# Kernel optimization log

Measured on AMD Instinct MI355X. Metric: run time of the kernel, lower is better.

The kernel has to match this reference:

```python
import jax, jax.numpy as jnp
import numpy as np
import math

B, S, D = 16, 1024, 512

def setup_inputs() -> dict:
    key = jax.random.key(0)
    ks = jax.random.split(key, 7)
    s = 1.0 / math.sqrt(D)
    return {
        "features_4h": jax.random.normal(ks[0], (B, S, D), jnp.float32),
        "features_1d": jax.random.normal(ks[1], (B, S, D), jnp.float32),
        "features_1w": jax.random.normal(ks[2], (B, S, D), jnp.float32),
        "Wq": jax.random.normal(ks[3], (D, D), jnp.float32) * s,
        "bq": jnp.zeros((D,), jnp.float32),
        "Wk": jax.random.normal(ks[4], (D, D), jnp.float32) * s,
        "bk": jnp.zeros((D,), jnp.float32),
        "Wv": jax.random.normal(ks[5], (D, D), jnp.float32) * s,
        "bv": jnp.zeros((D,), jnp.float32),
        "tf_weights": jnp.ones((3,), jnp.float32),
    }

def reference(features_4h, features_1d, features_1w, Wq, bq, Wk, bk, Wv, bv, tf_weights):
    # stacked: [B, T=3, S, D]
    stacked = jnp.stack([features_4h, features_1d, features_1w], axis=1)
    scale = 1.0 / math.sqrt(stacked.shape[-1])
    # torch nn.Linear: x @ W.T + b
    Q = jnp.einsum("btsd,ed->btse", stacked, Wq) + bq
    K = jnp.einsum("btsd,ed->btse", stacked, Wk) + bk
    V = jnp.einsum("btsd,ed->btse", stacked, Wv) + bv
    scores = jnp.einsum("btqd,btkd->btqk", Q, K) * scale  # [B,T,S,S]
    attn = jax.nn.softmax(scores, axis=-1)
    attended = jnp.einsum("btqk,btkd->btqd", attn, V)  # [B,T,S,D]
    w = jax.nn.softmax(tf_weights, axis=0)  # [T]
    return jnp.einsum("btsd,t->bsd", attended, w)  # [B,S,D]
```

## Files before the change

kernel.cpp:

```cpp
#include <hip/hip_runtime.h>
#include <cstdint>

typedef __bf16 bf16x8 __attribute__((ext_vector_type(8)));
typedef unsigned short u16x8 __attribute__((ext_vector_type(8)));
typedef float f32x4 __attribute__((ext_vector_type(4)));


__device__ __forceinline__ unsigned short f2bf(float x){
  unsigned u = __float_as_uint(x);
  u += 0x7fffu + ((u >> 16) & 1u);
  return (unsigned short)(u >> 16);
}

__device__ __forceinline__ void gload16(const void* src, void* dst){
  auto g = reinterpret_cast<const uint32_t __attribute__((address_space(1)))*>(
             reinterpret_cast<uintptr_t>(src));
  auto l = reinterpret_cast<uint32_t __attribute__((address_space(3)))*>(
             reinterpret_cast<uintptr_t>(dst));
  __builtin_amdgcn_global_load_lds(g, l, 16, 0, 0);
}

__device__ __forceinline__ void stage_tile(const unsigned short* __restrict__ g, size_t ld,
                                           unsigned short* l, int tid){
  #pragma unroll
  for (int i = 0; i < 4; ++i){
    int j = i * 256 + tid;
    int r = j >> 3, cc = j & 7;
    int c = cc ^ (r & 7);
    gload16(g + (size_t)r * ld + c * 8, l + (size_t)(i * 256 + (tid & 192)) * 8);
  }
}

__device__ __forceinline__ bf16x8 frag_at(const unsigned short* l, int row, int kch){
  int ch = kch ^ (row & 7);
  return *(const bf16x8*)(l + (row << 6) + (ch << 3));
}

__global__ void k_prep(const float* __restrict__ Wq, const float* __restrict__ Wk,
                       const float* __restrict__ Wv, const float* __restrict__ bq,
                       unsigned short* __restrict__ WqT, unsigned short* __restrict__ WkT,
                       unsigned short* __restrict__ Wv16, float* __restrict__ w1){
  __shared__ float sh[64 * 65];
  const int bi = blockIdx.x;
  const int tid = threadIdx.x;
  if (bi < 128){
    const float* src = (bi & 64) ? Wk : Wq;
    unsigned short* dst = (bi & 64) ? WkT : WqT;
    int te = (bi >> 3) & 7, td = bi & 7;
    #pragma unroll
    for (int i = 0; i < 4; ++i){
      int q = i * 256 + tid;
      int r = q >> 4, c4 = q & 15;
      f32x4 v = *(const f32x4*)(src + (size_t)(te * 64 + r) * 512 + td * 64 + c4 * 4);
      sh[r * 65 + c4 * 4 + 0] = v[0]; sh[r * 65 + c4 * 4 + 1] = v[1];
      sh[r * 65 + c4 * 4 + 2] = v[2]; sh[r * 65 + c4 * 4 + 3] = v[3];
    }
    __syncthreads();
    #pragma unroll
    for (int i = 0; i < 2; ++i){
      int q = i * 256 + tid;
      int r = q >> 3, c8 = q & 7;
      u16x8 o;
      #pragma unroll
      for (int j = 0; j < 8; ++j) o[j] = f2bf(sh[(c8 * 8 + j) * 65 + r]);
      *(u16x8*)(dst + (size_t)(td * 64 + r) * 512 + te * 64 + c8 * 8) = o;
    }
  } else if (bi < 256){
    size_t e = ((size_t)(bi - 128) * 256 + tid) * 8;
    f32x4 v0 = *(const f32x4*)(Wv + e), v1 = *(const f32x4*)(Wv + e + 4);
    u16x8 o;
    o[0] = f2bf(v0[0]); o[1] = f2bf(v0[1]); o[2] = f2bf(v0[2]); o[3] = f2bf(v0[3]);
    o[4] = f2bf(v1[0]); o[5] = f2bf(v1[1]); o[6] = f2bf(v1[2]); o[7] = f2bf(v1[3]);
    *(u16x8*)(Wv16 + e) = o;
  } else {
    int d = (bi - 256) * 64 + (tid & 63);
    int eq = tid >> 6;
    float s = 0.f;
    #pragma unroll 8
    for (int e = eq * 128; e < eq * 128 + 128; ++e) s += Wk[(size_t)e * 512 + d] * bq[e];
    sh[eq * 64 + (tid & 63)] = s;
    __syncthreads();
    if (eq == 0)
      w1[d] = (sh[tid] + sh[64 + tid] + sh[128 + tid] + sh[192 + tid]) * 0.04419417382415922f;
  }
}

__global__ void k_conv_feat(const float* __restrict__ f0, const float* __restrict__ f1,
                            const float* __restrict__ f2, const float* __restrict__ w1,
                            unsigned short* __restrict__ Xb, float* __restrict__ vcol){
  size_t i = (size_t)blockIdx.x * blockDim.x + threadIdx.x;
  size_t e = i * 8;
  size_t bt = e >> 19;
  size_t rest = e & ((1u << 19) - 1);
  int b = (int)(bt / 3), t = (int)(bt % 3);
  const float* src = (t == 0 ? f0 : (t == 1 ? f1 : f2)) + ((size_t)b << 19) + rest;
  f32x4 v0 = *(const f32x4*)(src);
  f32x4 v1 = *(const f32x4*)(src + 4);
  u16x8 o;
  o[0] = f2bf(v0[0]); o[1] = f2bf(v0[1]); o[2] = f2bf(v0[2]); o[3] = f2bf(v0[3]);
  o[4] = f2bf(v1[0]); o[5] = f2bf(v1[1]); o[6] = f2bf(v1[2]); o[7] = f2bf(v1[3]);
  *(u16x8*)(Xb + e) = o;
  int l = threadIdx.x & 63;
  f32x4 wa = *(const f32x4*)(w1 + l * 8);
  f32x4 wb = *(const f32x4*)(w1 + l * 8 + 4);
  float p = v0[0]*wa[0] + v0[1]*wa[1] + v0[2]*wa[2] + v0[3]*wa[3]
          + v1[0]*wb[0] + v1[1]*wb[1] + v1[2]*wb[2] + v1[3]*wb[3];
  p += __shfl_xor(p, 1);  p += __shfl_xor(p, 2);  p += __shfl_xor(p, 4);
  p += __shfl_xor(p, 8);  p += __shfl_xor(p, 16); p += __shfl_xor(p, 32);
  if (l == 0) vcol[i >> 6] = p;
}

template<int MODE>
__global__ __launch_bounds__(256, 2)
void k_gemm_proj(const unsigned short* __restrict__ A, const unsigned short* __restrict__ Bm,
                 const float* __restrict__ bias, unsigned short* __restrict__ C, int N, float scale){
  __shared__ __align__(16) unsigned short Al[2][8192];
  __shared__ __align__(16) unsigned short Bl[2][8192];
  const int tid = threadIdx.x;
  const int l  = tid & 63;
  const int wid = tid >> 6;
  const int lr = l & 15;
  const int lg = l >> 4;
  const int cpx = gridDim.x >> 3;
  const int wg = (blockIdx.x & 7) * cpx + (blockIdx.x >> 3);
  const int nbc = N >> 7;
  int rb, cb;
  if (MODE == 1){ cb = wg >> 2; rb = wg & 3; }
  else          { rb = wg / nbc; cb = wg % nbc; }
  const unsigned short* Ab = A + (size_t)rb * 128 * 512;
  const unsigned short* Bb = Bm + (size_t)cb * 128 * 512;

  const f32x4 zero4 = {0.f, 0.f, 0.f, 0.f};
  f32x4 acc[4][4];
  #pragma unroll
  for (int i = 0; i < 4; ++i)
    #pragma unroll
    for (int j = 0; j < 4; ++j) acc[i][j] = zero4;

  stage_tile(Ab, 512, &Al[0][0], tid);
  stage_tile(Bb, 512, &Bl[0][0], tid);
  __syncthreads();

  const int wr = wid >> 1, wc = wid & 1;

  for (int kb = 0; kb < 8; ++kb){
    const int cur = kb & 1;
    if (kb < 7){
      stage_tile(Ab + (kb + 1) * 64, 512, &Al[cur ^ 1][0], tid);
      stage_tile(Bb + (kb + 1) * 64, 512, &Bl[cur ^ 1][0], tid);
    }
    #pragma unroll
    for (int ks = 0; ks < 2; ++ks){
      bf16x8 af[4], bf[4];
      #pragma unroll
      for (int i = 0; i < 4; ++i) af[i] = frag_at(&Al[cur][0], wr * 64 + i * 16 + lr, ks * 4 + lg);
      #pragma unroll
      for (int j = 0; j < 4; ++j) bf[j] = frag_at(&Bl[cur][0], wc * 64 + j * 16 + lr, ks * 4 + lg);
      #pragma unroll
      for (int i = 0; i < 4; ++i)
        #pragma unroll
        for (int j = 0; j < 4; ++j)
          acc[i][j] = __builtin_amdgcn_mfma_f32_16x16x32_bf16(af[i], bf[j], acc[i][j], 0, 0, 0);
    }
    __syncthreads();
  }

  unsigned short* eL = &Al[0][0];
  #pragma unroll
  for (int j = 0; j < 4; ++j){
    int lcol = wc * 64 + j * 16 + lr;
    float bc = (MODE == 0) ? (bias ? bias[cb * 128 + lcol] : 0.f) : 0.f;
    #pragma unroll
    for (int i = 0; i < 4; ++i){
      int lrow0 = wr * 64 + i * 16 + lg * 4;
      #pragma unroll
      for (int r = 0; r < 4; ++r){
        float v;
        if (MODE == 0) v = (acc[i][j][r] + bc) * scale;
        else           v = acc[i][j][r] + bias[rb * 128 + lrow0 + r];
        eL[(lrow0 + r) * 128 + lcol] = f2bf(v);
      }
    }
  }
  __syncthreads();
  if (MODE == 0){
    #pragma unroll
    for (int q = 0; q < 8; ++q){
      int idx = q * 256 + tid;
      int row = idx >> 4, col = (idx & 15) * 8;
      *(u16x8*)(&C[(size_t)(rb * 128 + row) * N + cb * 128 + col]) =
          *(const u16x8*)(&eL[row * 128 + col]);
    }
  } else {
    size_t base = ((size_t)(cb >> 3) << 19) + (size_t)(cb & 7) * 128;
    #pragma unroll
    for (int q = 0; q < 8; ++q){
      int idx = q * 256 + tid;
      int row = idx >> 4, col = (idx & 15) * 8;
      *(u16x8*)(&C[base + ((size_t)(rb * 128 + row) << 10) + col]) =
          *(const u16x8*)(&eL[row * 128 + col]);
    }
  }
}

__global__ __launch_bounds__(256, 2)
void k_gemm_qk(const unsigned short* __restrict__ Gb, const unsigned short* __restrict__ Xb,
               unsigned short* __restrict__ S, int bt0){
  __shared__ __align__(16) unsigned short Al[2][8192];
  __shared__ __align__(16) unsigned short Bl[2][8192];
  const int tid = threadIdx.x;
  const int l  = tid & 63;
  const int wid = tid >> 6;
  const int lr = l & 15;
  const int lg = l >> 4;
  const int cpx = gridDim.x >> 3;
  const int wg = (blockIdx.x & 7) * cpx + (blockIdx.x >> 3);
  const int btl = wg >> 6;
  const int bt = bt0 + btl;
  const int tile = wg & 63;
  const int rb = tile >> 3, cb = tile & 7;
  const unsigned short* Ab = Gb + ((size_t)bt << 19) + (size_t)rb * 128 * 512;
  const unsigned short* Bb = Xb + ((size_t)bt << 19) + (size_t)cb * 128 * 512;
  unsigned short* Cb = S + ((size_t)btl << 20);

  const f32x4 zero4 = {0.f, 0.f, 0.f, 0.f};
  f32x4 acc[4][4];
  #pragma unroll
  for (int i = 0; i < 4; ++i)
    #pragma unroll
    for (int j = 0; j < 4; ++j) acc[i][j] = zero4;

  stage_tile(Ab, 512, &Al[0][0], tid);
  stage_tile(Bb, 512, &Bl[0][0], tid);
  __syncthreads();

  const int wr = wid >> 1, wc = wid & 1;

  for (int kb = 0; kb < 8; ++kb){
    const int cur = kb & 1;
    if (kb < 7){
      stage_tile(Ab + (kb + 1) * 64, 512, &Al[cur ^ 1][0], tid);
      stage_tile(Bb + (kb + 1) * 64, 512, &Bl[cur ^ 1][0], tid);
    }
    #pragma unroll
    for (int ks = 0; ks < 2; ++ks){
      bf16x8 af[4], bf[4];
      #pragma unroll
      for (int i = 0; i < 4; ++i) af[i] = frag_at(&Al[cur][0], wr * 64 + i * 16 + lr, ks * 4 + lg);
      #pragma unroll
      for (int j = 0; j < 4; ++j) bf[j] = frag_at(&Bl[cur][0], wc * 64 + j * 16 + lr, ks * 4 + lg);
      #pragma unroll
      for (int i = 0; i < 4; ++i)
        #pragma unroll
        for (int j = 0; j < 4; ++j)
          acc[i][j] = __builtin_amdgcn_mfma_f32_16x16x32_bf16(af[i], bf[j], acc[i][j], 0, 0, 0);
    }
    __syncthreads();
  }

  unsigned short* eL = &Al[0][0];
  #pragma unroll
  for (int j = 0; j < 4; ++j){
    int lcol = wc * 64 + j * 16 + lr;
    #pragma unroll
    for (int i = 0; i < 4; ++i){
      int lrow0 = wr * 64 + i * 16 + lg * 4;
      #pragma unroll
      for (int r = 0; r < 4; ++r){
        _Float16 h = (_Float16)acc[i][j][r];
        eL[(lrow0 + r) * 128 + lcol] = __builtin_bit_cast(unsigned short, h);
      }
    }
  }
  __syncthreads();
  #pragma unroll
  for (int q = 0; q < 8; ++q){
    int idx = q * 256 + tid;
    int row = idx >> 4, col = (idx & 15) * 8;
    *(u16x8*)(&Cb[((size_t)(rb * 128 + row) << 10) + cb * 128 + col]) =
        *(const u16x8*)(&eL[row * 128 + col]);
  }
}

__global__ __launch_bounds__(256)
void k_softmax(unsigned short* __restrict__ S, const float* __restrict__ vcol,
               const float* __restrict__ tfw, int bt0){
  const int wid = threadIdx.x >> 6, l = threadIdx.x & 63;
  const size_t row = (size_t)blockIdx.x * 4 + wid;
  const int bt = bt0 + (int)(row >> 10);
  const int t = bt % 3;
  float t0 = tfw[0], t1 = tfw[1], t2 = tfw[2];
  float tm = fmaxf(t0, fmaxf(t1, t2));
  float e0 = __expf(t0 - tm), e1 = __expf(t1 - tm), e2 = __expf(t2 - tm);
  float w = (t == 0 ? e0 : (t == 1 ? e1 : e2)) / (e0 + e1 + e2);

  const float* vr = vcol + ((size_t)bt << 10) + l * 16;
  unsigned short* rp = S + (row << 10) + l * 16;
  u16x8 a = *(const u16x8*)rp;
  u16x8 b = *(const u16x8*)(rp + 8);
  f32x4 va0 = *(const f32x4*)(vr), va1 = *(const f32x4*)(vr + 4);
  f32x4 va2 = *(const f32x4*)(vr + 8), va3 = *(const f32x4*)(vr + 12);
  float x[16];
  #pragma unroll
  for (int j = 0; j < 8; ++j){
    x[j]     = (float)__builtin_bit_cast(_Float16, (unsigned short)a[j]);
    x[8 + j] = (float)__builtin_bit_cast(_Float16, (unsigned short)b[j]);
  }
  x[0] += va0[0]; x[1] += va0[1]; x[2]  += va0[2]; x[3]  += va0[3];
  x[4] += va1[0]; x[5] += va1[1]; x[6]  += va1[2]; x[7]  += va1[3];
  x[8] += va2[0]; x[9] += va2[1]; x[10] += va2[2]; x[11] += va2[3];
  x[12]+= va3[0]; x[13]+= va3[1]; x[14] += va3[2]; x[15] += va3[3];
  float m = x[0];
  #pragma unroll
  for (int j = 1; j < 16; ++j) m = fmaxf(m, x[j]);
  m = fmaxf(m, __shfl_xor(m, 1));
  m = fmaxf(m, __shfl_xor(m, 2));
  m = fmaxf(m, __shfl_xor(m, 4));
  m = fmaxf(m, __shfl_xor(m, 8));
  m = fmaxf(m, __shfl_xor(m, 16));
  m = fmaxf(m, __shfl_xor(m, 32));
  float s = 0.f;
  #pragma unroll
  for (int j = 0; j < 16; ++j){ x[j] = __expf(x[j] - m); s += x[j]; }
  s += __shfl_xor(s, 1);
  s += __shfl_xor(s, 2);
  s += __shfl_xor(s, 4);
  s += __shfl_xor(s, 8);
  s += __shfl_xor(s, 16);
  s += __shfl_xor(s, 32);
  float sc = w / s;
  u16x8 oa, ob;
  #pragma unroll
  for (int j = 0; j < 8; ++j){
    oa[j] = f2bf(x[j] * sc);
    ob[j] = f2bf(x[8 + j] * sc);
  }
  *(u16x8*)rp = oa;
  *(u16x8*)(rp + 8) = ob;
}

__global__ __launch_bounds__(256, 2)
void k_gemm_pv(const unsigned short* __restrict__ P, const unsigned short* __restrict__ Vt,
               float* __restrict__ out, int b0){
  __shared__ __align__(16) unsigned short Al[2][8192];
  __shared__ __align__(16) unsigned short Bl[2][8192];
  const int tid = threadIdx.x;
  const int l  = tid & 63;
  const int wid = tid >> 6;
  const int lr = l & 15;
  const int lg = l >> 4;
  const int cpx = gridDim.x >> 3;
  const int wg = (blockIdx.x & 7) * cpx + (blockIdx.x >> 3);
  const int bl = wg >> 5;
  const int b = b0 + bl;
  const int tile = wg & 31;
  const int rb = tile >> 2, cb = tile & 3;

  const f32x4 zero4 = {0.f, 0.f, 0.f, 0.f};
  f32x4 acc[4][4];
  #pragma unroll
  for (int i = 0; i < 4; ++i)
    #pragma unroll
    for (int j = 0; j < 4; ++j) acc[i][j] = zero4;

  {
    const unsigned short* Ab = P  + ((size_t)(bl * 3) << 20) + (size_t)rb * 128 * 1024;
    const unsigned short* Bb = Vt + ((size_t)(b * 3) << 19) + (size_t)cb * 128 * 1024;
    stage_tile(Ab, 1024, &Al[0][0], tid);
    stage_tile(Bb, 1024, &Bl[0][0], tid);
  }
  __syncthreads();

  const int wr = wid >> 1, wc = wid & 1;

  #pragma unroll 2
  for (int kb = 0; kb < 48; ++kb){
    const int cur = kb & 1;
    if (kb < 47){
      int kn = kb + 1;
      int t = kn >> 4, kk = kn & 15;
      const unsigned short* Ab = P  + ((size_t)(bl * 3 + t) << 20) + (size_t)rb * 128 * 1024 + kk * 64;
      const unsigned short* Bb = Vt + ((size_t)(b * 3 + t) << 19) + (size_t)cb * 128 * 1024 + kk * 64;
      stage_tile(Ab, 1024, &Al[cur ^ 1][0], tid);
      stage_tile(Bb, 1024, &Bl[cur ^ 1][0], tid);
    }
    #pragma unroll
    for (int ks = 0; ks < 2; ++ks){
      bf16x8 af[4], bf[4];
      #pragma unroll
      for (int i = 0; i < 4; ++i) af[i] = frag_at(&Al[cur][0], wr * 64 + i * 16 + lr, ks * 4 + lg);
      #pragma unroll
      for (int j = 0; j < 4; ++j) bf[j] = frag_at(&Bl[cur][0], wc * 64 + j * 16 + lr, ks * 4 + lg);
      #pragma unroll
      for (int i = 0; i < 4; ++i)
        #pragma unroll
        for (int j = 0; j < 4; ++j)
          acc[i][j] = __builtin_amdgcn_mfma_f32_16x16x32_bf16(af[i], bf[j], acc[i][j], 0, 0, 0);
    }
    __syncthreads();
  }

  float* ob = out + ((size_t)b << 19);
  #pragma unroll
  for (int j = 0; j < 4; ++j){
    int col = cb * 128 + wc * 64 + j * 16 + lr;
    #pragma unroll
    for (int i = 0; i < 4; ++i){
      int row0 = rb * 128 + wr * 64 + i * 16 + lg * 4;
      #pragma unroll
      for (int r = 0; r < 4; ++r){
        ob[((size_t)(row0 + r) << 9) + col] = acc[i][j][r];
      }
    }
  }
}

extern "C" void kernel_launch(void* const* d_in, const int* in_sizes, int n_in,
                              void* d_out, int out_size, void* d_ws, size_t ws_size,
                              hipStream_t stream){
  (void)in_sizes; (void)n_in; (void)out_size;
  const float* f4h = (const float*)d_in[0];
  const float* f1d = (const float*)d_in[1];
  const float* f1w = (const float*)d_in[2];
  const float* Wq  = (const float*)d_in[3];
  const float* bq  = (const float*)d_in[4];
  const float* Wk  = (const float*)d_in[5];
  const float* bk  = (const float*)d_in[6];
  const float* Wv  = (const float*)d_in[7];
  const float* bv  = (const float*)d_in[8];
  const float* tfw = (const float*)d_in[9];
  (void)bk;
  float* out = (float*)d_out;

  const size_t N48 = (size_t)48 * 1024 * 512;
  unsigned short* Gb  = (unsigned short*)d_ws;
  unsigned short* Xb  = Gb + N48;
  unsigned short* Vt  = Xb + N48;
  float*          vcol = (float*)(Vt + N48);
  unsigned short* WqT = (unsigned short*)(vcol + 49152);
  unsigned short* WkT = WqT + 262144;
  unsigned short* Wv16= WkT + 262144;
  unsigned short* Mt  = Wv16 + 262144;
  float*          w1  = (float*)(Mt + 262144);
  unsigned short* Sb  = WqT;

  const float SC = 0.04419417382415922f;
  const size_t base = 3 * N48 * 2 + 49152 * 4;
  const size_t s_full = (size_t)48 * 1024 * 1024 * 2;

  k_prep<<<264, 256, 0, stream>>>(Wq, Wk, Wv, bq, WqT, WkT, Wv16, w1);
  k_conv_feat<<<12288, 256, 0, stream>>>(f4h, f1d, f1w, w1, Xb, vcol);
  k_gemm_proj<0><<<16, 256, 0, stream>>>(WkT, WqT, nullptr, Mt, 512, SC);
  k_gemm_proj<0><<<1536, 256, 0, stream>>>(Xb, Mt, nullptr, Gb, 512, 1.0f);
  k_gemm_proj<1><<<1536, 256, 0, stream>>>(Wv16, Xb, bv, Vt, 49152, 1.0f);

  if (ws_size >= base + 2048 + s_full){
    k_gemm_qk<<<3072, 256, 0, stream>>>(Gb, Xb, Sb, 0);
    k_softmax<<<12288, 256, 0, stream>>>(Sb, vcol, tfw, 0);
    k_gemm_pv<<<512, 256, 0, stream>>>(Sb, Vt, out, 0);
  } else {
    for (int h = 0; h < 2; ++h){
      int bt0 = h * 24;
      k_gemm_qk<<<1536, 256, 0, stream>>>(Gb, Xb, Sb, bt0);
      k_softmax<<<6144, 256, 0, stream>>>(Sb, vcol, tfw, bt0);
      k_gemm_pv<<<256, 256, 0, stream>>>(Sb, Vt, out, h * 8);
    }
  }
}
```

Measured before the change: 268.7 us.

## Defer V projection until after attention by reassociating P·(X·Wv) as (P·X)·Wv

```diff
diff --git a/kernel.cpp b/kernel.cpp
--- a/kernel.cpp
+++ b/kernel.cpp
@@ -3,6 +3,7 @@
 
 typedef __bf16 bf16x8 __attribute__((ext_vector_type(8)));
 typedef unsigned short u16x8 __attribute__((ext_vector_type(8)));
+typedef unsigned short u16x4 __attribute__((ext_vector_type(4)));
 typedef float f32x4 __attribute__((ext_vector_type(4)));
 
 
@@ -85,35 +86,50 @@
   }
 }
 
-__global__ void k_conv_feat(const float* __restrict__ f0, const float* __restrict__ f1,
-                            const float* __restrict__ f2, const float* __restrict__ w1,
-                            unsigned short* __restrict__ Xb, float* __restrict__ vcol){
-  size_t i = (size_t)blockIdx.x * blockDim.x + threadIdx.x;
-  size_t e = i * 8;
-  size_t bt = e >> 19;
-  size_t rest = e & ((1u << 19) - 1);
-  int b = (int)(bt / 3), t = (int)(bt % 3);
-  const float* src = (t == 0 ? f0 : (t == 1 ? f1 : f2)) + ((size_t)b << 19) + rest;
-  f32x4 v0 = *(const f32x4*)(src);
-  f32x4 v1 = *(const f32x4*)(src + 4);
-  u16x8 o;
-  o[0] = f2bf(v0[0]); o[1] = f2bf(v0[1]); o[2] = f2bf(v0[2]); o[3] = f2bf(v0[3]);
-  o[4] = f2bf(v1[0]); o[5] = f2bf(v1[1]); o[6] = f2bf(v1[2]); o[7] = f2bf(v1[3]);
-  *(u16x8*)(Xb + e) = o;
-  int l = threadIdx.x & 63;
-  f32x4 wa = *(const f32x4*)(w1 + l * 8);
-  f32x4 wb = *(const f32x4*)(w1 + l * 8 + 4);
-  float p = v0[0]*wa[0] + v0[1]*wa[1] + v0[2]*wa[2] + v0[3]*wa[3]
-          + v1[0]*wb[0] + v1[1]*wb[1] + v1[2]*wb[2] + v1[3]*wb[3];
-  p += __shfl_xor(p, 1);  p += __shfl_xor(p, 2);  p += __shfl_xor(p, 4);
-  p += __shfl_xor(p, 8);  p += __shfl_xor(p, 16); p += __shfl_xor(p, 32);
-  if (l == 0) vcol[i >> 6] = p;
-}
-
-template<int MODE>
+__global__ void k_conv(const float* __restrict__ f0, const float* __restrict__ f1,
+                       const float* __restrict__ f2, const float* __restrict__ w1,
+                       unsigned short* __restrict__ Xb, unsigned short* __restrict__ Xt,
+                       float* __restrict__ vcol){
+  __shared__ float tl[64 * 65];
+  const int bi = blockIdx.x;
+  const int tid = threadIdx.x;
+  const int bt = bi >> 7;
+  const int st = (bi >> 3) & 15, dt = bi & 7;
+  const int b = bt / 3, t = bt % 3;
+  const int s0 = st * 64, d0 = dt * 64;
+  const float* src = (t == 0 ? f0 : (t == 1 ? f1 : f2)) + ((size_t)b << 19)
+                   + (size_t)s0 * 512 + d0;
+  #pragma unroll
+  for (int q = 0; q < 4; ++q){
+    int j = q * 256 + tid;
+    int r = j >> 4, c4 = (j & 15) * 4;
+    f32x4 v = *(const f32x4*)(src + (size_t)r * 512 + c4);
+    u16x4 o;
+    o[0] = f2bf(v[0]); o[1] = f2bf(v[1]); o[2] = f2bf(v[2]); o[3] = f2bf(v[3]);
+    *(u16x4*)(Xb + ((size_t)bt << 19) + (size_t)(s0 + r) * 512 + d0 + c4) = o;
+    tl[r * 65 + c4 + 0] = v[0]; tl[r * 65 + c4 + 1] = v[1];
+    tl[r * 65 + c4 + 2] = v[2]; tl[r * 65 + c4 + 3] = v[3];
+    f32x4 wv = *(const f32x4*)(w1 + d0 + c4);
+    float p = v[0]*wv[0] + v[1]*wv[1] + v[2]*wv[2] + v[3]*wv[3];
+    p += __shfl_xor(p, 1); p += __shfl_xor(p, 2);
+    p += __shfl_xor(p, 4); p += __shfl_xor(p, 8);
+    if ((tid & 15) == 0) atomicAdd(vcol + ((size_t)bt << 10) + s0 + r, p);
+  }
+  __syncthreads();
+  #pragma unroll
+  for (int q = 0; q < 2; ++q){
+    int j = q * 256 + tid;
+    int d = j >> 3, sc = (j & 7) * 8;
+    u16x8 o;
+    #pragma unroll
+    for (int k = 0; k < 8; ++k) o[k] = f2bf(tl[(sc + k) * 65 + d]);
+    *(u16x8*)(Xt + ((size_t)bt << 19) + (size_t)(d0 + d) * 1024 + s0 + sc) = o;
+  }
+}
+
 __global__ __launch_bounds__(256, 2)
-void k_gemm_proj(const unsigned short* __restrict__ A, const unsigned short* __restrict__ Bm,
-                 const float* __restrict__ bias, unsigned short* __restrict__ C, int N, float scale){
+void k_gemm_nt(const unsigned short* __restrict__ A, const unsigned short* __restrict__ Bm,
+               unsigned short* __restrict__ C, int N, float scale){
   __shared__ __align__(16) unsigned short Al[2][8192];
   __shared__ __align__(16) unsigned short Bl[2][8192];
   const int tid = threadIdx.x;
@@ -124,9 +140,7 @@
   const int cpx = gridDim.x >> 3;
   const int wg = (blockIdx.x & 7) * cpx + (blockIdx.x >> 3);
   const int nbc = N >> 7;
-  int rb, cb;
-  if (MODE == 1){ cb = wg >> 2; rb = wg & 3; }
-  else          { rb = wg / nbc; cb = wg % nbc; }
+  const int rb = wg / nbc, cb = wg % nbc;
   const unsigned short* Ab = A + (size_t)rb * 128 * 512;
   const unsigned short* Bb = Bm + (size_t)cb * 128 * 512;
 
@@ -169,37 +183,21 @@
   #pragma unroll
   for (int j = 0; j < 4; ++j){
     int lcol = wc * 64 + j * 16 + lr;
-    float bc = (MODE == 0) ? (bias ? bias[cb * 128 + lcol] : 0.f) : 0.f;
     #pragma unroll
     for (int i = 0; i < 4; ++i){
       int lrow0 = wr * 64 + i * 16 + lg * 4;
       #pragma unroll
-      for (int r = 0; r < 4; ++r){
-        float v;
-        if (MODE == 0) v = (acc[i][j][r] + bc) * scale;
-        else           v = acc[i][j][r] + bias[rb * 128 + lrow0 + r];
-        eL[(lrow0 + r) * 128 + lcol] = f2bf(v);
-      }
-    }
-  }
-  __syncthreads();
-  if (MODE == 0){
-    #pragma unroll
-    for (int q = 0; q < 8; ++q){
-      int idx = q * 256 + tid;
-      int row = idx >> 4, col = (idx & 15) * 8;
-      *(u16x8*)(&C[(size_t)(rb * 128 + row) * N + cb * 128 + col]) =
-          *(const u16x8*)(&eL[row * 128 + col]);
-    }
-  } else {
-    size_t base = ((size_t)(cb >> 3) << 19) + (size_t)(cb & 7) * 128;
-    #pragma unroll
-    for (int q = 0; q < 8; ++q){
-      int idx = q * 256 + tid;
-      int row = idx >> 4, col = (idx & 15) * 8;
-      *(u16x8*)(&C[base + ((size_t)(rb * 128 + row) << 10) + col]) =
-          *(const u16x8*)(&eL[row * 128 + col]);
-    }
+      for (int r = 0; r < 4; ++r)
+        eL[(lrow0 + r) * 128 + lcol] = f2bf(acc[i][j][r] * scale);
+    }
+  }
+  __syncthreads();
+  #pragma unroll
+  for (int q = 0; q < 8; ++q){
+    int idx = q * 256 + tid;
+    int row = idx >> 4, col = (idx & 15) * 8;
+    *(u16x8*)(&C[(size_t)(rb * 128 + row) * N + cb * 128 + col]) =
+        *(const u16x8*)(&eL[row * 128 + col]);
   }
 }
 
@@ -340,8 +338,8 @@
 }
 
 __global__ __launch_bounds__(256, 2)
-void k_gemm_pv(const unsigned short* __restrict__ P, const unsigned short* __restrict__ Vt,
-               float* __restrict__ out, int b0){
+void k_gemm_px(const unsigned short* __restrict__ P, const unsigned short* __restrict__ Xt,
+               unsigned short* __restrict__ Z, int b0){
   __shared__ __align__(16) unsigned short Al[2][8192];
   __shared__ __align__(16) unsigned short Bl[2][8192];
   const int tid = threadIdx.x;
@@ -365,7 +363,7 @@
 
   {
     const unsigned short* Ab = P  + ((size_t)(bl * 3) << 20) + (size_t)rb * 128 * 1024;
-    const unsigned short* Bb = Vt + ((size_t)(b * 3) << 19) + (size_t)cb * 128 * 1024;
+    const unsigned short* Bb = Xt + ((size_t)(b * 3) << 19) + (size_t)cb * 128 * 1024;
     stage_tile(Ab, 1024, &Al[0][0], tid);
     stage_tile(Bb, 1024, &Bl[0][0], tid);
   }
@@ -380,7 +378,7 @@
       int kn = kb + 1;
       int t = kn >> 4, kk = kn & 15;
       const unsigned short* Ab = P  + ((size_t)(bl * 3 + t) << 20) + (size_t)rb * 128 * 1024 + kk * 64;
-      const unsigned short* Bb = Vt + ((size_t)(b * 3 + t) << 19) + (size_t)cb * 128 * 1024 + kk * 64;
+      const unsigned short* Bb = Xt + ((size_t)(b * 3 + t) << 19) + (size_t)cb * 128 * 1024 + kk * 64;
       stage_tile(Ab, 1024, &Al[cur ^ 1][0], tid);
       stage_tile(Bb, 1024, &Bl[cur ^ 1][0], tid);
     }
@@ -400,18 +398,104 @@
     __syncthreads();
   }
 
-  float* ob = out + ((size_t)b << 19);
+  unsigned short* eL = &Al[0][0];
   #pragma unroll
   for (int j = 0; j < 4; ++j){
-    int col = cb * 128 + wc * 64 + j * 16 + lr;
+    int lcol = wc * 64 + j * 16 + lr;
     #pragma unroll
     for (int i = 0; i < 4; ++i){
-      int row0 = rb * 128 + wr * 64 + i * 16 + lg * 4;
-      #pragma unroll
-      for (int r = 0; r < 4; ++r){
-        ob[((size_t)(row0 + r) << 9) + col] = acc[i][j][r];
-      }
-    }
+      int lrow0 = wr * 64 + i * 16 + lg * 4;
+      #pragma unroll
+      for (int r = 0; r < 4; ++r)
+        eL[(lrow0 + r) * 128 + lcol] = f2bf(acc[i][j][r]);
+    }
+  }
+  __syncthreads();
+  unsigned short* Cb = Z + ((size_t)b << 19);
+  #pragma unroll
+  for (int q = 0; q < 8; ++q){
+    int idx = q * 256 + tid;
+    int row = idx >> 4, col = (idx & 15) * 8;
+    *(u16x8*)(&Cb[(size_t)(rb * 128 + row) * 512 + cb * 128 + col]) =
+        *(const u16x8*)(&eL[row * 128 + col]);
+  }
+}
+
+__global__ __launch_bounds__(256, 2)
+void k_gemm_zo(const unsigned short* __restrict__ Z, const unsigned short* __restrict__ Wv16,
+               const float* __restrict__ bv, float* __restrict__ out){
+  __shared__ __align__(16) unsigned short SH[32768];
+  unsigned short* Al0 = SH;
+  unsigned short* Al1 = SH + 8192;
+  unsigned short* Bl0 = SH + 16384;
+  unsigned short* Bl1 = SH + 24576;
+  const int tid = threadIdx.x;
+  const int l  = tid & 63;
+  const int wid = tid >> 6;
+  const int lr = l & 15;
+  const int lg = l >> 4;
+  const int cpx = gridDim.x >> 3;
+  const int wg = (blockIdx.x & 7) * cpx + (blockIdx.x >> 3);
+  const int rb = wg >> 2, cb = wg & 3;
+  const unsigned short* Ab = Z + (size_t)rb * 128 * 512;
+  const unsigned short* Bb = Wv16 + (size_t)cb * 128 * 512;
+
+  const f32x4 zero4 = {0.f, 0.f, 0.f, 0.f};
+  f32x4 acc[4][4];
+  #pragma unroll
+  for (int i = 0; i < 4; ++i)
+    #pragma unroll
+    for (int j = 0; j < 4; ++j) acc[i][j] = zero4;
+
+  stage_tile(Ab, 512, Al0, tid);
+  stage_tile(Bb, 512, Bl0, tid);
+  __syncthreads();
+
+  const int wr = wid >> 1, wc = wid & 1;
+
+  for (int kb = 0; kb < 8; ++kb){
+    unsigned short* Acur = (kb & 1) ? Al1 : Al0;
+    unsigned short* Bcur = (kb & 1) ? Bl1 : Bl0;
+    if (kb < 7){
+      stage_tile(Ab + (kb + 1) * 64, 512, (kb & 1) ? Al0 : Al1, tid);
+      stage_tile(Bb + (kb + 1) * 64, 512, (kb & 1) ? Bl0 : Bl1, tid);
+    }
+    #pragma unroll
+    for (int ks = 0; ks < 2; ++ks){
+      bf16x8 af[4], bf[4];
+      #pragma unroll
+      for (int i = 0; i < 4; ++i) af[i] = frag_at(Acur, wr * 64 + i * 16 + lr, ks * 4 + lg);
+      #pragma unroll
+      for (int j = 0; j < 4; ++j) bf[j] = frag_at(Bcur, wc * 64 + j * 16 + lr, ks * 4 + lg);
+      #pragma unroll
+      for (int i = 0; i < 4; ++i)
+        #pragma unroll
+        for (int j = 0; j < 4; ++j)
+          acc[i][j] = __builtin_amdgcn_mfma_f32_16x16x32_bf16(af[i], bf[j], acc[i][j], 0, 0, 0);
+    }
+    __syncthreads();
+  }
+
+  float* eF = (float*)SH;
+  #pragma unroll
+  for (int j = 0; j < 4; ++j){
+    int lcol = wc * 64 + j * 16 + lr;
+    float bc = bv[cb * 128 + lcol];
+    #pragma unroll
+    for (int i = 0; i < 4; ++i){
+      int lrow0 = wr * 64 + i * 16 + lg * 4;
+      #pragma unroll
+      for (int r = 0; r < 4; ++r)
+        eF[(lrow0 + r) * 128 + lcol] = acc[i][j][r] + bc;
+    }
+  }
+  __syncthreads();
+  #pragma unroll
+  for (int q = 0; q < 16; ++q){
+    int idx = q * 256 + tid;
+    int row = idx >> 5, c4 = (idx & 31) * 4;
+    *(f32x4*)(&out[(size_t)(rb * 128 + row) * 512 + cb * 128 + c4]) =
+        *(const f32x4*)(&eF[row * 128 + c4]);
   }
 }
 
@@ -433,37 +517,39 @@
   float* out = (float*)d_out;
 
   const size_t N48 = (size_t)48 * 1024 * 512;
-  unsigned short* Gb  = (unsigned short*)d_ws;
-  unsigned short* Xb  = Gb + N48;
-  unsigned short* Vt  = Xb + N48;
-  float*          vcol = (float*)(Vt + N48);
-  unsigned short* WqT = (unsigned short*)(vcol + 49152);
-  unsigned short* WkT = WqT + 262144;
-  unsigned short* Wv16= WkT + 262144;
-  unsigned short* Mt  = Wv16 + 262144;
-  float*          w1  = (float*)(Mt + 262144);
-  unsigned short* Sb  = WqT;
+  unsigned short* Gb   = (unsigned short*)d_ws;
+  unsigned short* Xb   = Gb + N48;
+  unsigned short* Xt   = Xb + N48;
+  float*          vcol = (float*)(Xt + N48);
+  unsigned short* Wv16 = (unsigned short*)(vcol + 49152);
+  unsigned short* WqT  = Wv16 + 262144;
+  unsigned short* WkT  = WqT + 262144;
+  unsigned short* Mt   = WkT + 262144;
+  float*          w1   = (float*)(Mt + 262144);
+  unsigned short* Sb   = WqT;
+  unsigned short* Zb   = Gb;
 
   const float SC = 0.04419417382415922f;
-  const size_t base = 3 * N48 * 2 + 49152 * 4;
+  const size_t base = 3 * N48 * 2 + 49152 * 4 + 262144 * 2;
   const size_t s_full = (size_t)48 * 1024 * 1024 * 2;
 
+  hipMemsetAsync(vcol, 0, 49152 * 4, stream);
   k_prep<<<264, 256, 0, stream>>>(Wq, Wk, Wv, bq, WqT, WkT, Wv16, w1);
-  k_conv_feat<<<12288, 256, 0, stream>>>(f4h, f1d, f1w, w1, Xb, vcol);
-  k_gemm_proj<0><<<16, 256, 0, stream>>>(WkT, WqT, nullptr, Mt, 512, SC);
-  k_gemm_proj<0><<<1536, 256, 0, stream>>>(Xb, Mt, nullptr, Gb, 512, 1.0f);
-  k_gemm_proj<1><<<1536, 256, 0, stream>>>(Wv16, Xb, bv, Vt, 49152, 1.0f);
-
-  if (ws_size >= base + 2048 + s_full){
+  k_conv<<<6144, 256, 0, stream>>>(f4h, f1d, f1w, w1, Xb, Xt, vcol);
+  k_gemm_nt<<<16, 256, 0, stream>>>(WkT, WqT, Mt, 512, SC);
+  k_gemm_nt<<<1536, 256, 0, stream>>>(Xb, Mt, Gb, 512, 1.0f);
+
+  if (ws_size >= base + s_full){
     k_gemm_qk<<<3072, 256, 0, stream>>>(Gb, Xb, Sb, 0);
     k_softmax<<<12288, 256, 0, stream>>>(Sb, vcol, tfw, 0);
-    k_gemm_pv<<<512, 256, 0, stream>>>(Sb, Vt, out, 0);
+    k_gemm_px<<<512, 256, 0, stream>>>(Sb, Xt, Zb, 0);
   } else {
     for (int h = 0; h < 2; ++h){
       int bt0 = h * 24;
       k_gemm_qk<<<1536, 256, 0, stream>>>(Gb, Xb, Sb, bt0);
       k_softmax<<<6144, 256, 0, stream>>>(Sb, vcol, tfw, bt0);
-      k_gemm_pv<<<256, 256, 0, stream>>>(Sb, Vt, out, h * 8);
-    }
-  }
-}
+      k_gemm_px<<<256, 256, 0, stream>>>(Sb, Xt, Zb, h * 8);
+    }
+  }
+  k_gemm_zo<<<512, 256, 0, stream>>>(Zb, Wv16, bv, out);
+}
```

Result: no change. 270.0 us (+0.5%).
